# Kernel optimization log

Hardware: AMD Instinct MI355X
Metric: run time of the kernel (lower is better)

The kernel has to match this reference:

```python
import jax, jax.numpy as jnp
import numpy as np

N_NODES = 10000
N_EDGES = 320000
F_IN = 256
F_OUT = 256


def setup_inputs() -> dict:
    key = jax.random.key(0)
    k1, k2, k3 = jax.random.split(key, 3)
    X = jax.random.normal(k1, (N_NODES, F_IN), dtype=jnp.float32)
    # kaiming-normal init: std = sqrt(2 / fan_in)
    W = jax.random.normal(k2, (F_IN, F_OUT), dtype=jnp.float32) * np.float32(np.sqrt(2.0 / F_IN))
    edge_list = jax.random.randint(k3, (2, N_EDGES), 0, N_NODES, dtype=jnp.int64 if jax.config.jax_enable_x64 else jnp.int32)
    return {"X": X, "W": W, "edge_list": edge_list}


def reference(X, W, edge_list):
    # Faithful to the original: build dense adjacency from edge list
    # (duplicate edges collapse to 1 via set-semantics), add self-loops,
    # symmetric degree normalization D^{-1/2} A_hat D^{-1/2}, then X @ W, ReLU.
    n = X.shape[0]
    src, tgt = edge_list[0], edge_list[1]
    A = jnp.zeros((n, n), dtype=X.dtype).at[src, tgt].set(1.0)  # [N, N]
    A_hat = A + jnp.eye(n, dtype=X.dtype)
    deg = jnp.sum(A_hat, axis=0)                # column sums (in-degree + 1)
    d_inv_sqrt = 1.0 / jnp.sqrt(deg)            # diag(D)^-1 then sqrt == 1/sqrt(deg)
    # D_normed @ A_hat @ D_normed == d[:,None] * A_hat * d[None,:]
    norm_adj = A_hat * d_inv_sqrt[:, None] * d_inv_sqrt[None, :]
    z = norm_adj @ (X @ W)                      # [N, N] @ [N, F_out]
    return jax.nn.relu(z)
```

## Files before the change

### kernel.cpp

```cpp
#include <hip/hip_runtime.h>
#include <hip/hip_bf16.h>


constexpr int N = 10000;
constexpr int E = 320000;
constexpr int F = 256;
constexpr int DEGCAP = 96;
constexpr int GROWS = 25;
constexpr int NG = N / GROWS;
constexpr int BCAP = 12;
constexpr int REG_PB = NG * BCAP;

constexpr size_t OFF_DEG  = 0;
constexpr size_t OFF_CNT  = 40960;
constexpr size_t OFF_ADJ  = 81920;
constexpr size_t OFF_WT   = OFF_ADJ + 4ull * N * DEGCAP;
constexpr size_t OFF_H    = OFF_WT + 2ull * F * F;
constexpr size_t OFF_REG  = OFF_H + 2ull * N * F;
constexpr size_t OFF_PART = OFF_REG + 4ull * 1250 * REG_PB;

constexpr int BKT_BLKS  = E / 256;
constexpr int GEMM_BLKS = N / 16;

typedef short s8v __attribute__((ext_vector_type(8)));
typedef float f4v __attribute__((ext_vector_type(4)));
typedef unsigned u4v __attribute__((ext_vector_type(4)));

__device__ __forceinline__ float bf2f(unsigned short u) {
    union { unsigned u; float f; } c; c.u = (unsigned)u << 16; return c.f;
}
__device__ __forceinline__ unsigned short f2bf(float f) {
    union { __hip_bfloat16 b; unsigned short s; } c; c.b = __float2bfloat16(f); return c.s;
}

__global__ void k_pre(const float* __restrict__ W, unsigned short* __restrict__ Wt) {
    __shared__ unsigned short ls[4][F];
    int n0 = blockIdx.x * 4;
    int k = threadIdx.x;
    float4 v = *(const float4*)&W[k * F + n0];
    ls[0][k] = f2bf(v.x); ls[1][k] = f2bf(v.y);
    ls[2][k] = f2bf(v.z); ls[3][k] = f2bf(v.w);
    __syncthreads();
    int nn = threadIdx.x >> 6;
    int kk = (threadIdx.x & 63) * 4;
    uint2 o;
    o.x = (unsigned)ls[nn][kk]     | ((unsigned)ls[nn][kk + 1] << 16);
    o.y = (unsigned)ls[nn][kk + 2] | ((unsigned)ls[nn][kk + 3] << 16);
    *(uint2*)&Wt[(n0 + nn) * F + kk] = o;
}

__global__ void __launch_bounds__(256) k_bucket_gemm(
    const int* __restrict__ edges, int* __restrict__ region,
    const float* __restrict__ X, const unsigned short* __restrict__ Wt,
    unsigned short* __restrict__ H) {
    __shared__ int bkt[NG][BCAP];
    __shared__ int bcnt[NG];
    __shared__ unsigned short lsA[16][264];
    int tid = threadIdx.x;

    if (blockIdx.x < BKT_BLKS) {
        int probe = edges[2 * (tid & 63) + 1];
        bool is32 = __ballot(probe != 0) != 0ull;
        for (int i = tid; i < NG; i += 256) bcnt[i] = 0;
        int4 mone; mone.x = -1; mone.y = -1; mone.z = -1; mone.w = -1;
        int4* b4 = (int4*)&bkt[0][0];
        for (int i = tid; i < REG_PB / 4; i += 256) b4[i] = mone;
        __syncthreads();
        int e = blockIdx.x * 256 + tid;
        int s, t;
        if (is32) { s = edges[e];     t = edges[E + e]; }
        else      { s = edges[2 * e]; t = edges[2 * E + 2 * e]; }
        if ((unsigned)s < (unsigned)N && (unsigned)t < (unsigned)N) {
            int g = s / GROWS;
            int v = ((s - g * GROWS) << 14) | t;
            int pos = atomicAdd(&bcnt[g], 1);
            if (pos < BCAP) bkt[g][pos] = v;
        }
        __syncthreads();
        int4* dst = (int4*)(region + (size_t)blockIdx.x * REG_PB);
        for (int i = tid; i < REG_PB / 4; i += 256) dst[i] = b4[i];
        return;
    }
    int r0 = (blockIdx.x - BKT_BLKS) * 16;
    {
        int row = tid >> 4, seg = tid & 15;
        const float4* src = (const float4*)(X + (r0 + row) * F + seg * 16);
#pragma unroll
        for (int j = 0; j < 4; ++j) {
            float4 v = src[j];
            uint2 o;
            o.x = (unsigned)f2bf(v.x) | ((unsigned)f2bf(v.y) << 16);
            o.y = (unsigned)f2bf(v.z) | ((unsigned)f2bf(v.w) << 16);
            *(uint2*)&lsA[row][seg * 16 + j * 4] = o;
        }
    }
    __syncthreads();
    int lane = tid & 63, wv = tid >> 6;
    int m = lane & 15, q = lane >> 4;
    const s8v* B = (const s8v*)(Wt + m * F + q * 8);
    f4v acc[4] = {};
#pragma unroll
    for (int kk = 0; kk < 8; ++kk) {
        s8v af = *(const s8v*)&lsA[m][kk * 32 + q * 8];
#pragma unroll
        for (int tt = 0; tt < 4; ++tt) {
            int t = wv * 4 + tt;
            s8v bf = B[t * 512 + kk * 4];
            acc[tt] = __builtin_amdgcn_mfma_f32_16x16x32_bf16(af, bf, acc[tt], 0, 0, 0);
        }
    }
#pragma unroll
    for (int tt = 0; tt < 4; ++tt) {
        int col = (wv * 4 + tt) * 16 + m;
#pragma unroll
        for (int i = 0; i < 4; ++i)
            H[(r0 + q * 4 + i) * F + col] = f2bf(acc[tt][i]);
    }
}

__global__ void __launch_bounds__(512) k_fillscan(
    const int* __restrict__ region,
    int* __restrict__ adj, int* __restrict__ cnt, unsigned* __restrict__ part32) {
    __shared__ unsigned bmp[GROWS][320];
    __shared__ unsigned hist32[N / 4];
    int tid = threadIdx.x;
    {
        u4v z = {0u, 0u, 0u, 0u};
        u4v* z4 = (u4v*)&bmp[0][0];
        for (int i = tid; i < GROWS * 320 / 4; i += 512) z4[i] = z;
        u4v* h4 = (u4v*)hist32;
        for (int i = tid; i < N / 16; i += 512) h4[i] = z;
    }
    __syncthreads();

    int g = blockIdx.x;
    const u4v* reg4 = (const u4v*)region;
    for (int idx = tid; idx < BKT_BLKS * 3; idx += 512) {
        int j = idx / 3, q = idx - 3 * j;
        u4v v4 = reg4[(size_t)j * (REG_PB / 4) + g * 3 + q];
#pragma unroll
        for (int jj = 0; jj < 4; ++jj) {
            int v = (int)v4[jj];
            if (v >= 0) {
                int r = v >> 14;
                unsigned t = (unsigned)(v & 16383);
                atomicOr(&bmp[r][t >> 5], 1u << (t & 31));
            }
        }
    }
    __syncthreads();

    int wave = tid >> 6, lane = tid & 63;
    for (int r = wave; r < GROWS; r += 8) {
        int s = g * GROWS + r;
        const unsigned* row = bmp[r];
        unsigned w0 = row[lane];
        unsigned w1 = row[lane + 64];
        unsigned w2 = row[lane + 128];
        unsigned w3 = row[lane + 192];
        unsigned w4 = row[lane + 256];
        int pc = __popc(w0) + __popc(w1) + __popc(w2) + __popc(w3) + __popc(w4);
        int sc = pc;
#pragma unroll
        for (int d = 1; d < 64; d <<= 1) {
            int v = __shfl_up(sc, d);
            if (lane >= d) sc += v;
        }
        int o = sc - pc;
        if (lane == 63) cnt[s] = sc < DEGCAP ? sc : DEGCAP;
        int* arow = adj + s * DEGCAP;
        unsigned wvs[5] = {w0, w1, w2, w3, w4};
#pragma unroll
        for (int j = 0; j < 5; ++j) {
            unsigned w = wvs[j];
            int base = (j * 64 + lane) * 32;
            while (w) {
                int b = __ffs(w) - 1;
                w &= w - 1;
                int t = base + b;
                if (o < DEGCAP) arow[o] = t;
                ++o;
                atomicAdd(&hist32[t >> 2], 1u << ((t & 3) * 8));
            }
        }
    }
    __syncthreads();
    {
        u4v* src = (u4v*)hist32;
        u4v* dst = (u4v*)(part32 + (size_t)g * (N / 4));
        for (int i = tid; i < N / 16; i += 512) dst[i] = src[i];
    }
}

__global__ void k_deg(const unsigned* __restrict__ part32, int* __restrict__ deg) {
    int j2 = blockIdx.x * blockDim.x + threadIdx.x;
    if (j2 >= N / 4) return;
    int s0 = 1, s1 = 1, s2 = 1, s3 = 1;
#pragma unroll 8
    for (int b = 0; b < NG; ++b) {
        unsigned w = part32[(size_t)b * (N / 4) + j2];
        s0 += w & 255; s1 += (w >> 8) & 255; s2 += (w >> 16) & 255; s3 += w >> 24;
    }
    int4 o; o.x = s0; o.y = s1; o.z = s2; o.w = s3;
    *(int4*)&deg[j2 * 4] = o;
}

#define ACC8(hv, dv)                                          \
    p0 += dv * bf2f((unsigned short)(hv.x & 0xFFFF));         \
    p1 += dv * bf2f((unsigned short)(hv.x >> 16));            \
    p2 += dv * bf2f((unsigned short)(hv.y & 0xFFFF));         \
    p3 += dv * bf2f((unsigned short)(hv.y >> 16));            \
    p4 += dv * bf2f((unsigned short)(hv.z & 0xFFFF));         \
    p5 += dv * bf2f((unsigned short)(hv.z >> 16));            \
    p6 += dv * bf2f((unsigned short)(hv.w & 0xFFFF));         \
    p7 += dv * bf2f((unsigned short)(hv.w >> 16));

__global__ void k_gather(const int* __restrict__ adj, const int* __restrict__ cnt,
                         const int* __restrict__ deg,
                         const unsigned short* __restrict__ H,
                         float* __restrict__ out) {
    int wave = threadIdx.x >> 6;
    int lane = threadIdx.x & 63;
    int s = blockIdx.x * 4 + wave;
    int half = lane >> 5, hl = lane & 31;
    const uint4* H16 = (const uint4*)H;
    float ds = rsqrtf((float)deg[s]);
    int c = cnt[s]; if (c > DEGCAP) c = DEGCAP;
    const int* a = adj + s * DEGCAP;
    int tl = 0; float dl = 0.0f;
    if (lane < c) { tl = a[lane]; dl = rsqrtf((float)deg[tl]); }

    uint4 hs = H16[s * 32 + hl];
    float p0, p1, p2, p3, p4, p5, p6, p7;
    {
        float w = half ? 0.0f : ds;
        p0 = w * bf2f((unsigned short)(hs.x & 0xFFFF));
        p1 = w * bf2f((unsigned short)(hs.x >> 16));
        p2 = w * bf2f((unsigned short)(hs.y & 0xFFFF));
        p3 = w * bf2f((unsigned short)(hs.y >> 16));
        p4 = w * bf2f((unsigned short)(hs.z & 0xFFFF));
        p5 = w * bf2f((unsigned short)(hs.z >> 16));
        p6 = w * bf2f((unsigned short)(hs.w & 0xFFFF));
        p7 = w * bf2f((unsigned short)(hs.w >> 16));
    }
    int cc = c < 64 ? c : 64;
    for (int i = 0; i < cc; i += 8) {
        int i0 = i + half, i1 = i + 2 + half, i2 = i + 4 + half, i3 = i + 6 + half;
        int t0 = __shfl(tl, i0), t1 = __shfl(tl, i1);
        int t2 = __shfl(tl, i2), t3 = __shfl(tl, i3);
        float d0 = __shfl(dl, i0), d1 = __shfl(dl, i1);
        float d2 = __shfl(dl, i2), d3 = __shfl(dl, i3);
        uint4 h0 = H16[t0 * 32 + hl];
        uint4 h1 = H16[t1 * 32 + hl];
        uint4 h2 = H16[t2 * 32 + hl];
        uint4 h3 = H16[t3 * 32 + hl];
        ACC8(h0, d0) ACC8(h1, d1) ACC8(h2, d2) ACC8(h3, d3)
    }
    for (int i = 64; i < c; ++i) {
        int t = a[i];
        float d = half ? 0.0f : rsqrtf((float)deg[t]);
        uint4 h = H16[t * 32 + hl];
        ACC8(h, d)
    }
    p0 += __shfl(p0, lane ^ 32); p1 += __shfl(p1, lane ^ 32);
    p2 += __shfl(p2, lane ^ 32); p3 += __shfl(p3, lane ^ 32);
    p4 += __shfl(p4, lane ^ 32); p5 += __shfl(p5, lane ^ 32);
    p6 += __shfl(p6, lane ^ 32); p7 += __shfl(p7, lane ^ 32);
    p0 = fmaxf(p0 * ds, 0.0f); p1 = fmaxf(p1 * ds, 0.0f);
    p2 = fmaxf(p2 * ds, 0.0f); p3 = fmaxf(p3 * ds, 0.0f);
    p4 = fmaxf(p4 * ds, 0.0f); p5 = fmaxf(p5 * ds, 0.0f);
    p6 = fmaxf(p6 * ds, 0.0f); p7 = fmaxf(p7 * ds, 0.0f);
    float4 o;
    if (half) { o.x = p4; o.y = p5; o.z = p6; o.w = p7; }
    else      { o.x = p0; o.y = p1; o.z = p2; o.w = p3; }
    ((float4*)out)[s * 64 + hl * 2 + half] = o;
}

extern "C" void kernel_launch(void* const* d_in, const int* in_sizes, int n_in,
                              void* d_out, int out_size, void* d_ws, size_t ws_size,
                              hipStream_t stream) {
    const float* X = (const float*)d_in[0];
    const float* W = (const float*)d_in[1];
    const int* edges = (const int*)d_in[2];

    char* ws = (char*)d_ws;
    int* deg           = (int*)(ws + OFF_DEG);
    int* cnt           = (int*)(ws + OFF_CNT);
    int* adj           = (int*)(ws + OFF_ADJ);
    unsigned short* Wt = (unsigned short*)(ws + OFF_WT);
    unsigned short* H  = (unsigned short*)(ws + OFF_H);
    int* region        = (int*)(ws + OFF_REG);
    unsigned* part32   = (unsigned*)(ws + OFF_PART);

    k_pre<<<64, 256, 0, stream>>>(W, Wt);
    k_bucket_gemm<<<BKT_BLKS + GEMM_BLKS, 256, 0, stream>>>(edges, region, X, Wt, H);
    k_fillscan<<<NG, 512, 0, stream>>>(region, adj, cnt, part32);
    k_deg<<<(N / 4 + 255) / 256, 256, 0, stream>>>(part32, deg);
    k_gather<<<N / 4, 256, 0, stream>>>(adj, cnt, deg, H, (float*)d_out);
}
```

Baseline: 137.1 us.

## Coarsen edge bucketing per block and enlarge GEMM row tiles

```diff
diff --git a/kernel.cpp b/kernel.cpp
--- a/kernel.cpp
+++ b/kernel.cpp
@@ -8,8 +8,12 @@
 constexpr int DEGCAP = 96;
 constexpr int GROWS = 25;
 constexpr int NG = N / GROWS;
-constexpr int BCAP = 12;
+constexpr int EPB = 2048;
+constexpr int BCAP = 28;
 constexpr int REG_PB = NG * BCAP;
+
+constexpr int BKT_BLKS  = (E + EPB - 1) / EPB;
+constexpr int GEMM_BLKS = (N + 31) / 32;
 
 constexpr size_t OFF_DEG  = 0;
 constexpr size_t OFF_CNT  = 40960;
@@ -17,10 +21,7 @@
 constexpr size_t OFF_WT   = OFF_ADJ + 4ull * N * DEGCAP;
 constexpr size_t OFF_H    = OFF_WT + 2ull * F * F;
 constexpr size_t OFF_REG  = OFF_H + 2ull * N * F;
-constexpr size_t OFF_PART = OFF_REG + 4ull * 1250 * REG_PB;
-
-constexpr int BKT_BLKS  = E / 256;
-constexpr int GEMM_BLKS = N / 16;
+constexpr size_t OFF_PART = OFF_REG + 4ull * BKT_BLKS * REG_PB;
 
 typedef short s8v __attribute__((ext_vector_type(8)));
 typedef float f4v __attribute__((ext_vector_type(4)));
@@ -49,72 +50,82 @@
     *(uint2*)&Wt[(n0 + nn) * F + kk] = o;
 }
 
-__global__ void __launch_bounds__(256) k_bucket_gemm(
+__global__ void __launch_bounds__(512) k_bucket_gemm(
     const int* __restrict__ edges, int* __restrict__ region,
     const float* __restrict__ X, const unsigned short* __restrict__ Wt,
     unsigned short* __restrict__ H) {
-    __shared__ int bkt[NG][BCAP];
-    __shared__ int bcnt[NG];
-    __shared__ unsigned short lsA[16][264];
+    __shared__ union U {
+        struct { int bkt[NG][BCAP]; int bcnt[NG]; } b;
+        unsigned short lsA[32][264];
+    } sh;
     int tid = threadIdx.x;
 
     if (blockIdx.x < BKT_BLKS) {
         int probe = edges[2 * (tid & 63) + 1];
         bool is32 = __ballot(probe != 0) != 0ull;
-        for (int i = tid; i < NG; i += 256) bcnt[i] = 0;
+        for (int i = tid; i < NG; i += 512) sh.b.bcnt[i] = 0;
         int4 mone; mone.x = -1; mone.y = -1; mone.z = -1; mone.w = -1;
-        int4* b4 = (int4*)&bkt[0][0];
-        for (int i = tid; i < REG_PB / 4; i += 256) b4[i] = mone;
+        int4* b4 = (int4*)&sh.b.bkt[0][0];
+        for (int i = tid; i < REG_PB / 4; i += 512) b4[i] = mone;
         __syncthreads();
-        int e = blockIdx.x * 256 + tid;
-        int s, t;
-        if (is32) { s = edges[e];     t = edges[E + e]; }
-        else      { s = edges[2 * e]; t = edges[2 * E + 2 * e]; }
-        if ((unsigned)s < (unsigned)N && (unsigned)t < (unsigned)N) {
-            int g = s / GROWS;
-            int v = ((s - g * GROWS) << 14) | t;
-            int pos = atomicAdd(&bcnt[g], 1);
-            if (pos < BCAP) bkt[g][pos] = v;
+#pragma unroll
+        for (int k = 0; k < EPB / 512; ++k) {
+            int e = blockIdx.x * EPB + k * 512 + tid;
+            if (e >= E) break;
+            int s, t;
+            if (is32) { s = edges[e];     t = edges[E + e]; }
+            else      { s = edges[2 * e]; t = edges[2 * E + 2 * e]; }
+            if ((unsigned)s < (unsigned)N && (unsigned)t < (unsigned)N) {
+                int g = s / GROWS;
+                int v = ((s - g * GROWS) << 14) | t;
+                int pos = atomicAdd(&sh.b.bcnt[g], 1);
+                if (pos < BCAP) sh.b.bkt[g][pos] = v;
+            }
         }
         __syncthreads();
         int4* dst = (int4*)(region + (size_t)blockIdx.x * REG_PB);
-        for (int i = tid; i < REG_PB / 4; i += 256) dst[i] = b4[i];
+        for (int i = tid; i < REG_PB / 4; i += 512) dst[i] = b4[i];
         return;
     }
-    int r0 = (blockIdx.x - BKT_BLKS) * 16;
+    int r0 = (blockIdx.x - BKT_BLKS) * 32;
     {
         int row = tid >> 4, seg = tid & 15;
-        const float4* src = (const float4*)(X + (r0 + row) * F + seg * 16);
-#pragma unroll
-        for (int j = 0; j < 4; ++j) {
-            float4 v = src[j];
-            uint2 o;
-            o.x = (unsigned)f2bf(v.x) | ((unsigned)f2bf(v.y) << 16);
-            o.y = (unsigned)f2bf(v.z) | ((unsigned)f2bf(v.w) << 16);
-            *(uint2*)&lsA[row][seg * 16 + j * 4] = o;
+        if (r0 + row < N) {
+            const float4* src = (const float4*)(X + (r0 + row) * F + seg * 16);
+#pragma unroll
+            for (int j = 0; j < 4; ++j) {
+                float4 v = src[j];
+                uint2 o;
+                o.x = (unsigned)f2bf(v.x) | ((unsigned)f2bf(v.y) << 16);
+                o.y = (unsigned)f2bf(v.z) | ((unsigned)f2bf(v.w) << 16);
+                *(uint2*)&sh.lsA[row][seg * 16 + j * 4] = o;
+            }
         }
     }
     __syncthreads();
     int lane = tid & 63, wv = tid >> 6;
+    int sl = wv >> 2;
+    int cg = wv & 3;
+    if (r0 + sl * 16 >= N) return;
     int m = lane & 15, q = lane >> 4;
     const s8v* B = (const s8v*)(Wt + m * F + q * 8);
     f4v acc[4] = {};
 #pragma unroll
     for (int kk = 0; kk < 8; ++kk) {
-        s8v af = *(const s8v*)&lsA[m][kk * 32 + q * 8];
+        s8v af = *(const s8v*)&sh.lsA[sl * 16 + m][kk * 32 + q * 8];
 #pragma unroll
         for (int tt = 0; tt < 4; ++tt) {
-            int t = wv * 4 + tt;
+            int t = cg * 4 + tt;
             s8v bf = B[t * 512 + kk * 4];
             acc[tt] = __builtin_amdgcn_mfma_f32_16x16x32_bf16(af, bf, acc[tt], 0, 0, 0);
         }
     }
 #pragma unroll
     for (int tt = 0; tt < 4; ++tt) {
-        int col = (wv * 4 + tt) * 16 + m;
+        int col = (cg * 4 + tt) * 16 + m;
 #pragma unroll
         for (int i = 0; i < 4; ++i)
-            H[(r0 + q * 4 + i) * F + col] = f2bf(acc[tt][i]);
+            H[(r0 + sl * 16 + q * 4 + i) * F + col] = f2bf(acc[tt][i]);
     }
 }
 
@@ -135,9 +146,9 @@
 
     int g = blockIdx.x;
     const u4v* reg4 = (const u4v*)region;
-    for (int idx = tid; idx < BKT_BLKS * 3; idx += 512) {
-        int j = idx / 3, q = idx - 3 * j;
-        u4v v4 = reg4[(size_t)j * (REG_PB / 4) + g * 3 + q];
+    for (int idx = tid; idx < BKT_BLKS * (BCAP / 4); idx += 512) {
+        int j = idx / (BCAP / 4), q = idx - (BCAP / 4) * j;
+        u4v v4 = reg4[(size_t)j * (REG_PB / 4) + g * (BCAP / 4) + q];
 #pragma unroll
         for (int jj = 0; jj < 4; ++jj) {
             int v = (int)v4[jj];
@@ -293,7 +304,7 @@
     unsigned* part32   = (unsigned*)(ws + OFF_PART);
 
     k_pre<<<64, 256, 0, stream>>>(W, Wt);
-    k_bucket_gemm<<<BKT_BLKS + GEMM_BLKS, 256, 0, stream>>>(edges, region, X, Wt, H);
+    k_bucket_gemm<<<BKT_BLKS + GEMM_BLKS, 512, 0, stream>>>(edges, region, X, Wt, H);
     k_fillscan<<<NG, 512, 0, stream>>>(region, adj, cnt, part32);
     k_deg<<<(N / 4 + 255) / 256, 256, 0, stream>>>(part32, deg);
     k_gather<<<N / 4, 256, 0, stream>>>(adj, cnt, deg, H, (float*)d_out);
```

New measurement: 127.0 us. 1.08x faster.
